# Kernel optimization log

Measured on AMD Instinct MI355X. Metric: run time of the kernel, lower is better.

## Reference

```python
import math
import jax, jax.numpy as jnp
import numpy as np

B, S, D_MODEL, H = 8, 1024, 512, 8
HEAD = D_MODEL // H
MAX_REL = 16


def rel_index(length_q, length_k):
    # clipped relative-position index matrix [Lq, Lk] in [0, 2*MAX_REL]
    rq = jnp.arange(length_q)
    rk = jnp.arange(length_k)
    dist = rk[None, :] - rq[:, None]
    return jnp.clip(dist, -MAX_REL, MAX_REL) + MAX_REL


def setup_inputs() -> dict:
    key = jax.random.key(0)
    ks = jax.random.split(key, 13)
    sc = 1.0 / math.sqrt(D_MODEL)
    inp = {
        "query": jax.random.normal(ks[0], (B, S, D_MODEL), jnp.float32),
        "key": jax.random.normal(ks[1], (B, S, D_MODEL), jnp.float32),
        "value": jax.random.normal(ks[2], (B, S, D_MODEL), jnp.float32),
        "Wq": jax.random.normal(ks[3], (D_MODEL, D_MODEL), jnp.float32) * sc,
        "bq": jnp.zeros((D_MODEL,), jnp.float32),
        "Wk": jax.random.normal(ks[4], (D_MODEL, D_MODEL), jnp.float32) * sc,
        "bk": jnp.zeros((D_MODEL,), jnp.float32),
        "Wv": jax.random.normal(ks[5], (D_MODEL, D_MODEL), jnp.float32) * sc,
        "bv": jnp.zeros((D_MODEL,), jnp.float32),
        "Wo": jax.random.normal(ks[6], (D_MODEL, D_MODEL), jnp.float32) * sc,
        "bo": jnp.zeros((D_MODEL,), jnp.float32),
        "rel_k_table": jax.random.normal(ks[7], (2 * MAX_REL + 1, HEAD), jnp.float32),
        "rel_v_table": jax.random.normal(ks[8], (2 * MAX_REL + 1, HEAD), jnp.float32),
    }
    return inp


def reference(query, key, value, Wq, bq, Wk, bk, Wv, bv, Wo, bo, rel_k_table, rel_v_table):
    b, s, d = query.shape
    # input projections (torch Linear: x @ W.T + b)
    q = query @ Wq.T + bq  # [B,S,D]
    k = key @ Wk.T + bk
    v = value @ Wv.T + bv
    # split heads: [B,H,S,HEAD]
    qh = q.reshape(b, s, H, HEAD).transpose(0, 2, 1, 3)
    kh = k.reshape(b, s, H, HEAD).transpose(0, 2, 1, 3)
    vh = v.reshape(b, s, H, HEAD).transpose(0, 2, 1, 3)
    # content-content scores
    attn1 = jnp.einsum("bhqd,bhkd->bhqk", qh, kh)
    # content-position scores via gathered relative embeddings [S,S,HEAD]
    idx = rel_index(s, s)
    rk = rel_k_table[idx]
    attn2 = jnp.einsum("bhqd,qkd->bhqk", qh, rk)
    # NOTE: original code scales by sqrt(batch_size), reproduced faithfully
    scale = math.sqrt(float(B))
    attn = jax.nn.softmax((attn1 + attn2) / scale, axis=-1)
    # values: content + relative-position value term
    w1 = jnp.einsum("bhqk,bhkd->bhqd", attn, vh)
    rv = rel_v_table[idx]
    w2 = jnp.einsum("bhqk,qkd->bhqd", attn, rv)
    x = (w1 + w2).transpose(0, 2, 1, 3).reshape(b * s, d)
    return x @ Wo.T + bo
```

## Files before the change

### kernel.cpp

```cpp
#include <hip/hip_runtime.h>

typedef unsigned short u16;
typedef float f32x4 __attribute__((ext_vector_type(4)));
typedef float f32x16 __attribute__((ext_vector_type(16)));
typedef __bf16 bf16x8 __attribute__((ext_vector_type(8)));

#define MFMA16(a, b, c) __builtin_amdgcn_mfma_f32_16x16x32_bf16((a), (b), (c), 0, 0, 0)
#define MFMA32(a, b, c) __builtin_amdgcn_mfma_f32_32x32x16_bf16((a), (b), (c), 0, 0, 0)

#define B_ 8
#define H_ 8
#define S_ 1024

__device__ __forceinline__ u16 f2bf(float f) {
  unsigned u = __float_as_uint(f);
  return (u16)((u + 0x7fffu + ((u >> 16) & 1u)) >> 16);
}
__device__ __forceinline__ unsigned cvtpk(float a, float b) {
  unsigned r;
  asm("v_cvt_pk_bf16_f32 %0, %1, %2" : "=v"(r) : "v"(a), "v"(b));
  return r;
}
__device__ __forceinline__ void plswap(unsigned& a, unsigned& b) {
  asm("v_permlane32_swap_b32 %0, %1" : "+v"(a), "+v"(b));
}
__device__ __forceinline__ void gload16(const void* g, void* l) {
  __builtin_amdgcn_global_load_lds((__attribute__((address_space(1))) const void*)g,
                                   (__attribute__((address_space(3))) void*)l, 16, 0, 0);
}

__global__ void __launch_bounds__(256) convAll(const float* __restrict__ q, const float* __restrict__ k,
                                               const float* __restrict__ v, const float* __restrict__ Wq,
                                               const float* __restrict__ Wk, const float* __restrict__ Wv,
                                               const float* __restrict__ Wo, const float* __restrict__ relk,
                                               u16* __restrict__ dq, u16* __restrict__ dk, u16* __restrict__ dv,
                                               u16* __restrict__ dWq, u16* __restrict__ dWk, u16* __restrict__ dWv,
                                               u16* __restrict__ dWo, u16* __restrict__ drelk) {
  const int bid = blockIdx.x;
  const float* s; u16* d; size_t off;
  if (bid < 12288) {
    size_t i4 = (size_t)bid * 256 + threadIdx.x;
    int tsel = (int)(i4 >> 20);
    off = (i4 & 1048575) << 2;
    s = tsel == 0 ? q : (tsel == 1 ? k : v);
    d = tsel == 0 ? dq : (tsel == 1 ? dk : dv);
  } else {
    size_t i = ((size_t)(bid - 12288) * 256 + threadIdx.x) << 2;
    if (i >= 1050688) return;
    if (i < 262144)       { s = Wq; d = dWq; off = i; }
    else if (i < 524288)  { s = Wk; d = dWk; off = i - 262144; }
    else if (i < 786432)  { s = Wv; d = dWv; off = i - 524288; }
    else if (i < 1048576) { s = Wo; d = dWo; off = i - 786432; }
    else                  { s = relk; d = drelk; off = i - 1048576; }
  }
  float4 f = *(const float4*)(s + off);
  uint2 o;
  o.x = cvtpk(f.x, f.y);
  o.y = cvtpk(f.z, f.w);
  *(uint2*)(d + off) = o;
}

__global__ void __launch_bounds__(256) qkv_gemm(const u16* __restrict__ Xq, const u16* __restrict__ Xk,
                                                const u16* __restrict__ Xv, const u16* __restrict__ Wqb,
                                                const u16* __restrict__ Wkb, const u16* __restrict__ Wvb,
                                                const float* __restrict__ bq, const float* __restrict__ bk,
                                                const float* __restrict__ bv, u16* __restrict__ Qh,
                                                u16* __restrict__ Kh, u16* __restrict__ Vt) {
  __shared__ u16 As[128 * 64];
  __shared__ u16 Bs[128 * 64];
  const int seg = blockIdx.x >> 8, bid = blockIdx.x & 255;
  const u16* A = seg == 0 ? Xq : (seg == 1 ? Xk : Xv);
  const u16* W = seg == 0 ? Wqb : (seg == 1 ? Wkb : Wvb);
  const float* bias = seg == 0 ? bq : (seg == 1 ? bk : bv);
  const int tid = threadIdx.x, lane = tid & 63, wid = tid >> 6;
  const int c = lane & 15, g = lane >> 4;
  const int bm = bid >> 2, bn = bid & 3;
  const int m0 = bm << 7, n0 = bn << 7;
  const int wrow = (wid >> 1) << 6, wcol = (wid & 1) << 6;

  const f32x4 ZF = {0.f, 0.f, 0.f, 0.f};
  f32x4 acc[4][4];
#pragma unroll
  for (int i = 0; i < 4; ++i)
#pragma unroll
    for (int j = 0; j < 4; ++j) acc[i][j] = ZF;

  for (int kt = 0; kt < 512; kt += 64) {
    __syncthreads();
#pragma unroll
    for (int i = 0; i < 4; ++i) {
      int Lb = ((wid << 2) | i) << 10;
      int L = Lb + lane * 16;
      int row = L >> 7;
      int off = (L & 127) ^ ((row & 7) << 4);
      gload16((const char*)A + ((((size_t)(m0 + row)) << 9) + kt) * 2 + off, (char*)As + Lb);
      gload16((const char*)W + ((((size_t)(n0 + row)) << 9) + kt) * 2 + off, (char*)Bs + Lb);
    }
    __syncthreads();
#pragma unroll
    for (int kk = 0; kk < 2; ++kk) {
      bf16x8 af[4], bfr[4];
#pragma unroll
      for (int rt = 0; rt < 4; ++rt) {
        int row = wrow + (rt << 4) + c;
        af[rt] = *(const bf16x8*)((const char*)As + row * 128 + (((kk << 6) | (g << 4)) ^ ((row & 7) << 4)));
      }
#pragma unroll
      for (int ct = 0; ct < 4; ++ct) {
        int row = wcol + (ct << 4) + c;
        bfr[ct] = *(const bf16x8*)((const char*)Bs + row * 128 + (((kk << 6) | (g << 4)) ^ ((row & 7) << 4)));
      }
#pragma unroll
      for (int rt = 0; rt < 4; ++rt)
#pragma unroll
        for (int ct = 0; ct < 4; ++ct) acc[rt][ct] = MFMA16(af[rt], bfr[ct], acc[rt][ct]);
    }
  }

#pragma unroll
  for (int rt = 0; rt < 4; ++rt)
#pragma unroll
    for (int ct = 0; ct < 4; ++ct) {
      int n = n0 + wcol + (ct << 4) + c;
      float bv2 = bias[n];
      if (seg == 2) {
        int b2 = m0 >> 10;
        int sbase = (m0 & 1023) + wrow + (rt << 4) + (g << 2);
        int h2 = n >> 6, d2 = n & 63;
        uint2 o;
        o.x = cvtpk(acc[rt][ct][0] + bv2, acc[rt][ct][1] + bv2);
        o.y = cvtpk(acc[rt][ct][2] + bv2, acc[rt][ct][3] + bv2);
        *(uint2*)(Vt + ((((size_t)((b2 << 3) + h2) << 6) + d2) << 10) + sbase) = o;
      } else {
        u16* out = seg == 0 ? Qh : Kh;
#pragma unroll
        for (int r = 0; r < 4; ++r) {
          int m = m0 + wrow + (rt << 4) + (g << 2) + r;
          int b = m >> 10, s = m & 1023, h = n >> 6, d = n & 63;
          out[(((((size_t)(b * H_ + h)) << 10) + s) << 6) + d] = f2bf(acc[rt][ct][r] + bv2);
        }
      }
    }
}

__global__ void __launch_bounds__(256) gemm_out(const u16* __restrict__ A, const u16* __restrict__ W,
                                                const float* __restrict__ bias, float* __restrict__ out) {
  __shared__ u16 As[128 * 64];
  __shared__ u16 Bs[128 * 64];
  const int tid = threadIdx.x, lane = tid & 63, wid = tid >> 6;
  const int c = lane & 15, g = lane >> 4;
  const int bm = blockIdx.x >> 2, bn = blockIdx.x & 3;
  const int m0 = bm << 7, n0 = bn << 7;
  const int wrow = (wid >> 1) << 6, wcol = (wid & 1) << 6;

  const f32x4 ZF = {0.f, 0.f, 0.f, 0.f};
  f32x4 acc[4][4];
#pragma unroll
  for (int i = 0; i < 4; ++i)
#pragma unroll
    for (int j = 0; j < 4; ++j) acc[i][j] = ZF;

  for (int kt = 0; kt < 512; kt += 64) {
    __syncthreads();
#pragma unroll
    for (int i = 0; i < 4; ++i) {
      int Lb = ((wid << 2) | i) << 10;
      int L = Lb + lane * 16;
      int row = L >> 7;
      int off = (L & 127) ^ ((row & 7) << 4);
      gload16((const char*)A + ((((size_t)(m0 + row)) << 9) + kt) * 2 + off, (char*)As + Lb);
      gload16((const char*)W + ((((size_t)(n0 + row)) << 9) + kt) * 2 + off, (char*)Bs + Lb);
    }
    __syncthreads();
#pragma unroll
    for (int kk = 0; kk < 2; ++kk) {
      bf16x8 af[4], bfr[4];
#pragma unroll
      for (int rt = 0; rt < 4; ++rt) {
        int row = wrow + (rt << 4) + c;
        af[rt] = *(const bf16x8*)((const char*)As + row * 128 + (((kk << 6) | (g << 4)) ^ ((row & 7) << 4)));
      }
#pragma unroll
      for (int ct = 0; ct < 4; ++ct) {
        int row = wcol + (ct << 4) + c;
        bfr[ct] = *(const bf16x8*)((const char*)Bs + row * 128 + (((kk << 6) | (g << 4)) ^ ((row & 7) << 4)));
      }
#pragma unroll
      for (int rt = 0; rt < 4; ++rt)
#pragma unroll
        for (int ct = 0; ct < 4; ++ct) acc[rt][ct] = MFMA16(af[rt], bfr[ct], acc[rt][ct]);
    }
  }

#pragma unroll
  for (int rt = 0; rt < 4; ++rt)
#pragma unroll
    for (int ct = 0; ct < 4; ++ct) {
      int n = n0 + wcol + (ct << 4) + c;
      float bv = bias[n];
#pragma unroll
      for (int r = 0; r < 4; ++r) {
        int m = m0 + wrow + (rt << 4) + (g << 2) + r;
        out[(((size_t)m) << 9) + n] = acc[rt][ct][r] + bv;
      }
    }
}

__global__ void __launch_bounds__(256) flash_kernel(const u16* __restrict__ Qh, const u16* __restrict__ Kh,
                                                    const u16* __restrict__ Vt, const u16* __restrict__ relkb,
                                                    const float* __restrict__ relv, u16* __restrict__ Xout) {
  __shared__ u16 Ks[2][64 * 64];
  __shared__ u16 Vs[2][64 * 64];
  __shared__ float qrelS[128 * 33];
  __shared__ u16 Pband[128 * 32];
  __shared__ float rv32S[64];
  __shared__ float2 normS[128];

  const int tid = threadIdx.x, lane = tid & 63, wid = tid >> 6;
  const int c32 = lane & 31, hi = lane >> 5;
  const int swz = ((blockIdx.x & 7) << 6) | (blockIdx.x >> 3);
  const int bh = swz >> 3, qt = swz & 7;
  const int qbase = qt << 7;
  const size_t rowbase = ((size_t)bh) << 10;
  const int wavebase = wid << 5;
  const int qloc = wavebase + c32;
  const float K1 = 0.51013619f;
  const float C0 = 24.0f;

#define STAGE(buf, kt_) do { \
    const int k64_ = (kt_) << 6; \
    _Pragma("unroll") \
    for (int i_ = 0; i_ < 2; ++i_) { \
      int Lb_ = ((wid << 1) | i_) << 10; \
      int L_ = Lb_ + lane * 16; \
      int row_ = L_ >> 7; \
      int off_ = (L_ & 127) ^ ((row_ & 7) << 4); \
      gload16((const char*)Kh + ((rowbase + k64_ + row_) << 7) + off_, (char*)Ks[buf] + Lb_); \
      gload16((const char*)Vt + ((((size_t)bh << 6) + row_) << 11) + (k64_ << 1) + off_, (char*)Vs[buf] + Lb_); \
    } \
  } while (0)

  STAGE(0, 0);

  ((uint4*)Pband)[tid] = uint4{0, 0, 0, 0};
  ((uint4*)Pband)[tid + 256] = uint4{0, 0, 0, 0};
  if (tid < 64) rv32S[tid] = relv[2048 + tid];

  {
    const int c = lane & 15, g = lane >> 4;
    const f32x4 ZF4 = {0.f, 0.f, 0.f, 0.f};
#pragma unroll
    for (int hf = 0; hf < 2; ++hf) {
      const int q16 = wavebase + (hf << 4) + c;
      const u16* qp = Qh + ((rowbase + qbase + q16) << 6);
      bf16x8 qa0 = *(const bf16x8*)(qp + (g << 3));
      bf16x8 qa1 = *(const bf16x8*)(qp + 32 + (g << 3));
#pragma unroll
      for (int t = 0; t < 3; ++t) {
        int rr = t * 16 + c; if (rr > 32) rr = 32;
        f32x4 qr = ZF4;
        qr = MFMA16(*(const bf16x8*)(relkb + (rr << 6) + (g << 3)), qa0, qr);
        qr = MFMA16(*(const bf16x8*)(relkb + (rr << 6) + 32 + (g << 3)), qa1, qr);
#pragma unroll
        for (int j = 0; j < 4; ++j) {
          int r = t * 16 + (g << 2) + j;
          if (r < 33) qrelS[q16 * 33 + r] = qr[j] * K1 - C0;
        }
      }
    }
  }

  bf16x8 qb[4];
  {
    const u16* qp = Qh + ((rowbase + qbase + qloc) << 6);
#pragma unroll
    for (int ks = 0; ks < 4; ++ks) qb[ks] = *(const bf16x8*)(qp + (ks << 4) + (hi << 3));
  }

  __syncthreads();

  const float bias_lo = qrelS[qloc * 33 + 0];
  const float bias_hi = qrelS[qloc * 33 + 32];

  int off2[2][4];
#pragma unroll
  for (int mt = 0; mt < 2; ++mt) {
    int row = (mt << 5) + c32;
#pragma unroll
    for (int ks = 0; ks < 4; ++ks)
      off2[mt][ks] = row * 128 + ((((ks << 5) | (hi << 4))) ^ ((row & 7) << 4));
  }

  const f32x16 Z16 = {0.f,0.f,0.f,0.f,0.f,0.f,0.f,0.f,0.f,0.f,0.f,0.f,0.f,0.f,0.f,0.f};
  f32x16 acc0 = Z16, acc1 = Z16;
  float lsum = 0.f, lowsum = 0.f, psum = 0.f;

  for (int kt = 0; kt < 16; ++kt) {
    const int cur = kt & 1;
    if (kt < 15) STAGE(cur ^ 1, kt + 1);

    f32x16 sA = Z16, sB = Z16;
#pragma unroll
    for (int ks = 0; ks < 4; ++ks) {
      bf16x8 ka0 = *(const bf16x8*)((const char*)Ks + (cur << 13) + off2[0][ks]);
      bf16x8 ka1 = *(const bf16x8*)((const char*)Ks + (cur << 13) + off2[1][ks]);
      sA = MFMA32(ka0, qb[ks], sA);
      sB = MFMA32(ka1, qb[ks], sB);
    }

    const int D0 = (kt << 6) - qbase;
    if (D0 >= 192) {
      float t0 = 0.f;
#pragma unroll
      for (int r = 0; r < 16; ++r) {
        float pe = __builtin_amdgcn_exp2f(fmaf(sA[r], K1, bias_hi)); sA[r] = pe; t0 += pe;
        float pf = __builtin_amdgcn_exp2f(fmaf(sB[r], K1, bias_hi)); sB[r] = pf; t0 += pf;
      }
      lsum += t0;
    } else if (D0 <= -128) {
      float t0 = 0.f;
#pragma unroll
      for (int r = 0; r < 16; ++r) {
        float pe = __builtin_amdgcn_exp2f(fmaf(sA[r], K1, bias_lo)); sA[r] = pe; t0 += pe;
        float pf = __builtin_amdgcn_exp2f(fmaf(sB[r], K1, bias_lo)); sB[r] = pf; t0 += pf;
      }
      lsum += t0; lowsum += t0;
    } else {
      const int base = D0 - qloc + (hi << 2);
#pragma unroll
      for (int mt = 0; mt < 2; ++mt) {
        f32x16& s = mt ? sB : sA;
#pragma unroll
        for (int r = 0; r < 16; ++r) {
          int dlt = base + (mt << 5) + (r & 3) + ((r >> 2) << 3);
          int idx = dlt < -16 ? 0 : (dlt > 16 ? 32 : dlt + 16);
          float pe = __builtin_amdgcn_exp2f(fmaf(s[r], K1, qrelS[qloc * 33 + idx]));
          s[r] = pe;
          lsum += pe;
          if (dlt <= -16) lowsum += pe;
          else if (dlt < 16) { psum += pe; Pband[(qloc << 5) + dlt + 16] = f2bf(pe); }
        }
      }
    }

    unsigned uA[8], uB[8];
#pragma unroll
    for (int j = 0; j < 8; ++j) {
      uA[j] = cvtpk(sA[2 * j], sA[2 * j + 1]);
      uB[j] = cvtpk(sB[2 * j], sB[2 * j + 1]);
    }
    bf16x8 pa[4];
#pragma unroll
    for (int ks = 0; ks < 4; ++ks) {
      int jb = (ks & 1) << 2;
      unsigned w0, w1, w2, w3;
      if (ks < 2) { w0 = uA[jb]; w2 = uA[jb + 2]; w1 = uA[jb + 1]; w3 = uA[jb + 3]; }
      else        { w0 = uB[jb]; w2 = uB[jb + 2]; w1 = uB[jb + 1]; w3 = uB[jb + 3]; }
      plswap(w0, w2);
      plswap(w1, w3);
      uint4 t4{w0, w1, w2, w3};
      pa[ks] = __builtin_bit_cast(bf16x8, t4);
    }

#pragma unroll
    for (int ks = 0; ks < 4; ++ks) {
      bf16x8 vb0 = *(const bf16x8*)((const char*)Vs + (cur << 13) + off2[0][ks]);
      bf16x8 vb1 = *(const bf16x8*)((const char*)Vs + (cur << 13) + off2[1][ks]);
      acc0 = MFMA32(pa[ks], vb0, acc0);
      acc1 = MFMA32(pa[ks], vb1, acc1);
    }
    __syncthreads();
  }

  lsum += __shfl_xor(lsum, 32);
  lowsum += __shfl_xor(lowsum, 32);
  psum += __shfl_xor(psum, 32);
  const float inv = 1.f / lsum;
  const float hsum = lsum - lowsum - psum;
  if (lane < 32) {
    Pband[qloc << 5] = f2bf(lowsum);
    normS[qloc] = float2{inv, hsum};
  }
  __syncthreads();
  u16* rvT = (u16*)qrelS;
  for (int i = tid; i < 2048; i += 256) rvT[i] = f2bf(relv[((i & 31) << 6) + (i >> 5)]);
  __syncthreads();

#pragma unroll
  for (int ks2 = 0; ks2 < 2; ++ks2) {
    bf16x8 pf = *(const bf16x8*)(Pband + (qloc << 5) + (ks2 << 4) + (hi << 3));
    bf16x8 rv0 = *(const bf16x8*)(rvT + (c32 << 5) + (ks2 << 4) + (hi << 3));
    bf16x8 rv1 = *(const bf16x8*)(rvT + ((32 + c32) << 5) + (ks2 << 4) + (hi << 3));
    acc0 = MFMA32(pf, rv0, acc0);
    acc1 = MFMA32(pf, rv1, acc1);
  }

  const int b = bh >> 3, h = bh & 7;
  const float rvA = rv32S[c32], rvB = rv32S[32 + c32];
#pragma unroll
  for (int r = 0; r < 16; ++r) {
    int qw = wavebase + (r & 3) + ((r >> 2) << 3) + (hi << 2);
    float2 nh = normS[qw];
    size_t orow = ((((size_t)b << 10) + (qbase + qw)) << 9) + (h << 6);
    Xout[orow + c32]      = f2bf((acc0[r] + nh.y * rvA) * nh.x);
    Xout[orow + 32 + c32] = f2bf((acc1[r] + nh.y * rvB) * nh.x);
  }
#undef STAGE
}

extern "C" void kernel_launch(void* const* d_in, const int* in_sizes, int n_in,
                              void* d_out, int out_size, void* d_ws, size_t ws_size,
                              hipStream_t stream) {
  (void)in_sizes; (void)n_in; (void)out_size; (void)ws_size;
  const float* query = (const float*)d_in[0];
  const float* key   = (const float*)d_in[1];
  const float* value = (const float*)d_in[2];
  const float* Wq = (const float*)d_in[3];
  const float* bq = (const float*)d_in[4];
  const float* Wk = (const float*)d_in[5];
  const float* bk = (const float*)d_in[6];
  const float* Wv = (const float*)d_in[7];
  const float* bv = (const float*)d_in[8];
  const float* Wo = (const float*)d_in[9];
  const float* bo = (const float*)d_in[10];
  const float* relk = (const float*)d_in[11];
  const float* relv = (const float*)d_in[12];

  char* ws = (char*)d_ws;
  u16*   Xq    = (u16*)(ws + 0);
  u16*   Xk    = (u16*)(ws + 8388608);
  u16*   Xv    = (u16*)(ws + 16777216);
  u16*   Wqb   = (u16*)(ws + 25165824);
  u16*   Wkb   = (u16*)(ws + 25690112);
  u16*   Wvb   = (u16*)(ws + 26214400);
  u16*   Wob   = (u16*)(ws + 26738688);
  u16*   relkb = (u16*)(ws + 27262976);
  u16*   Qh    = (u16*)(ws + 27271168);
  u16*   Kh    = (u16*)(ws + 35659776);
  u16*   Vt    = (u16*)(ws + 52436992);
  u16*   Xout  = (u16*)(ws + 70262784);

  convAll<<<13315, 256, 0, stream>>>(query, key, value, Wq, Wk, Wv, Wo, relk,
                                     Xq, Xk, Xv, Wqb, Wkb, Wvb, Wob, relkb);
  qkv_gemm<<<768, 256, 0, stream>>>(Xq, Xk, Xv, Wqb, Wkb, Wvb, bq, bk, bv, Qh, Kh, Vt);
  flash_kernel<<<512, 256, 0, stream>>>(Qh, Kh, Vt, relkb, relv, Xout);
  gemm_out<<<256, 256, 0, stream>>>(Xout, Wob, bo, (float*)d_out);
}
```

Measured before the change: 102.7 us.

## Double flash attention block query tile to 256 rows and repack K/V LDS layout

The flash kernel now runs 512 threads (8 waves) per block covering 256 query rows, halving the grid to 256 blocks so each staged K/V tile is shared by twice as many query rows. The K/V staging is rewritten so each wave loads a 1 KB chunk laid out in MFMA operand order, which removes the XOR swizzle and precomputed offsets in favour of lane-linear LDS reads. The band-classification thresholds become per-wave. The trade-off is larger LDS use and fewer blocks, which may lower occupancy and leave some compute units underfilled.

```diff
diff --git a/kernel.cpp b/kernel.cpp
--- a/kernel.cpp
+++ b/kernel.cpp
@@ -206,21 +206,21 @@
     }
 }
 
-__global__ void __launch_bounds__(256) flash_kernel(const u16* __restrict__ Qh, const u16* __restrict__ Kh,
+__global__ void __launch_bounds__(512) flash_kernel(const u16* __restrict__ Qh, const u16* __restrict__ Kh,
                                                     const u16* __restrict__ Vt, const u16* __restrict__ relkb,
                                                     const float* __restrict__ relv, u16* __restrict__ Xout) {
   __shared__ u16 Ks[2][64 * 64];
   __shared__ u16 Vs[2][64 * 64];
-  __shared__ float qrelS[128 * 33];
-  __shared__ u16 Pband[128 * 32];
+  __shared__ float qrelS[256 * 33];
+  __shared__ u16 Pband[256 * 32];
   __shared__ float rv32S[64];
-  __shared__ float2 normS[128];
+  __shared__ float2 normS[256];
 
   const int tid = threadIdx.x, lane = tid & 63, wid = tid >> 6;
   const int c32 = lane & 31, hi = lane >> 5;
-  const int swz = ((blockIdx.x & 7) << 6) | (blockIdx.x >> 3);
-  const int bh = swz >> 3, qt = swz & 7;
-  const int qbase = qt << 7;
+  const int swz = ((blockIdx.x & 7) << 5) | (blockIdx.x >> 3);
+  const int bh = swz >> 2, qt = swz & 3;
+  const int qbase = qt << 8;
   const size_t rowbase = ((size_t)bh) << 10;
   const int wavebase = wid << 5;
   const int qloc = wavebase + c32;
@@ -229,21 +229,17 @@
 
 #define STAGE(buf, kt_) do { \
     const int k64_ = (kt_) << 6; \
-    _Pragma("unroll") \
-    for (int i_ = 0; i_ < 2; ++i_) { \
-      int Lb_ = ((wid << 1) | i_) << 10; \
-      int L_ = Lb_ + lane * 16; \
-      int row_ = L_ >> 7; \
-      int off_ = (L_ & 127) ^ ((row_ & 7) << 4); \
-      gload16((const char*)Kh + ((rowbase + k64_ + row_) << 7) + off_, (char*)Ks[buf] + Lb_); \
-      gload16((const char*)Vt + ((((size_t)bh << 6) + row_) << 11) + (k64_ << 1) + off_, (char*)Vs[buf] + Lb_); \
-    } \
+    gload16((const char*)Kh + ((rowbase + k64_ + ((wid & 1) << 5) + c32) << 7) + ((wid >> 1) << 5) + (hi << 4), \
+            (char*)Ks[buf] + (wid << 10)); \
+    gload16((const char*)Vt + ((((size_t)(bh << 6)) + ((wid & 1) << 5) + c32) << 11) + \
+                ((k64_ + ((wid >> 1) << 4) + (hi << 3)) << 1), \
+            (char*)Vs[buf] + (wid << 10)); \
   } while (0)
 
   STAGE(0, 0);
 
   ((uint4*)Pband)[tid] = uint4{0, 0, 0, 0};
-  ((uint4*)Pband)[tid + 256] = uint4{0, 0, 0, 0};
+  ((uint4*)Pband)[tid + 512] = uint4{0, 0, 0, 0};
   if (tid < 64) rv32S[tid] = relv[2048 + tid];
 
   {
@@ -281,15 +277,7 @@
 
   const float bias_lo = qrelS[qloc * 33 + 0];
   const float bias_hi = qrelS[qloc * 33 + 32];
-
-  int off2[2][4];
-#pragma unroll
-  for (int mt = 0; mt < 2; ++mt) {
-    int row = (mt << 5) + c32;
-#pragma unroll
-    for (int ks = 0; ks < 4; ++ks)
-      off2[mt][ks] = row * 128 + ((((ks << 5) | (hi << 4))) ^ ((row & 7) << 4));
-  }
+  const int lb16 = lane << 4;
 
   const f32x16 Z16 = {0.f,0.f,0.f,0.f,0.f,0.f,0.f,0.f,0.f,0.f,0.f,0.f,0.f,0.f,0.f,0.f};
   f32x16 acc0 = Z16, acc1 = Z16;
@@ -302,14 +290,14 @@
     f32x16 sA = Z16, sB = Z16;
 #pragma unroll
     for (int ks = 0; ks < 4; ++ks) {
-      bf16x8 ka0 = *(const bf16x8*)((const char*)Ks + (cur << 13) + off2[0][ks]);
-      bf16x8 ka1 = *(const bf16x8*)((const char*)Ks + (cur << 13) + off2[1][ks]);
+      bf16x8 ka0 = *(const bf16x8*)((const char*)Ks[cur] + (((ks << 1) | 0) << 10) + lb16);
+      bf16x8 ka1 = *(const bf16x8*)((const char*)Ks[cur] + (((ks << 1) | 1) << 10) + lb16);
       sA = MFMA32(ka0, qb[ks], sA);
       sB = MFMA32(ka1, qb[ks], sB);
     }
 
-    const int D0 = (kt << 6) - qbase;
-    if (D0 >= 192) {
+    const int E = (kt << 6) - qbase - wavebase;
+    if (E >= 48) {
       float t0 = 0.f;
 #pragma unroll
       for (int r = 0; r < 16; ++r) {
@@ -317,7 +305,7 @@
         float pf = __builtin_amdgcn_exp2f(fmaf(sB[r], K1, bias_hi)); sB[r] = pf; t0 += pf;
       }
       lsum += t0;
-    } else if (D0 <= -128) {
+    } else if (E <= -80) {
       float t0 = 0.f;
 #pragma unroll
       for (int r = 0; r < 16; ++r) {
@@ -326,7 +314,7 @@
       }
       lsum += t0; lowsum += t0;
     } else {
-      const int base = D0 - qloc + (hi << 2);
+      const int base = E - c32 + (hi << 2);
 #pragma unroll
       for (int mt = 0; mt < 2; ++mt) {
         f32x16& s = mt ? sB : sA;
@@ -364,8 +352,8 @@
 
 #pragma unroll
     for (int ks = 0; ks < 4; ++ks) {
-      bf16x8 vb0 = *(const bf16x8*)((const char*)Vs + (cur << 13) + off2[0][ks]);
-      bf16x8 vb1 = *(const bf16x8*)((const char*)Vs + (cur << 13) + off2[1][ks]);
+      bf16x8 vb0 = *(const bf16x8*)((const char*)Vs[cur] + (((ks << 1) | 0) << 10) + lb16);
+      bf16x8 vb1 = *(const bf16x8*)((const char*)Vs[cur] + (((ks << 1) | 1) << 10) + lb16);
       acc0 = MFMA32(pa[ks], vb0, acc0);
       acc1 = MFMA32(pa[ks], vb1, acc1);
     }
@@ -383,7 +371,7 @@
   }
   __syncthreads();
   u16* rvT = (u16*)qrelS;
-  for (int i = tid; i < 2048; i += 256) rvT[i] = f2bf(relv[((i & 31) << 6) + (i >> 5)]);
+  for (int i = tid; i < 2048; i += 512) rvT[i] = f2bf(relv[((i & 31) << 6) + (i >> 5)]);
   __syncthreads();
 
 #pragma unroll
@@ -443,6 +431,6 @@
   convAll<<<13315, 256, 0, stream>>>(query, key, value, Wq, Wk, Wv, Wo, relk,
                                      Xq, Xk, Xv, Wqb, Wkb, Wvb, Wob, relkb);
   qkv_gemm<<<768, 256, 0, stream>>>(Xq, Xk, Xv, Wqb, Wkb, Wvb, bq, bk, bv, Qh, Kh, Vt);
-  flash_kernel<<<512, 256, 0, stream>>>(Qh, Kh, Vt, relkb, relv, Xout);
+  flash_kernel<<<256, 512, 0, stream>>>(Qh, Kh, Vt, relkb, relv, Xout);
   gemm_out<<<256, 256, 0, stream>>>(Xout, Wob, bo, (float*)d_out);
 }
```

Result: slower. 105.5 us (+2.7%).
